# Performance work log

Measured on AMD Instinct MI355X. Metric: run time of the kernel, lower is better.

Reference implementation:

```python
import jax, jax.numpy as jnp
import numpy as np

D = 512      # d_model
H = 8        # n_heads
DH = D // H  # d_head
WIN = 128    # window radius
FF = 4 * D   # ffn hidden
B, T = 4, 2048
EPS = 1e-5


def _ln(x, g, b):
    mu = jnp.mean(x, axis=-1, keepdims=True)
    var = jnp.mean((x - mu) ** 2, axis=-1, keepdims=True)
    return (x - mu) * jax.lax.rsqrt(var + EPS) * g + b


def _rope(x):
    # standard rotate-half RoPE over the full d_model dim (applied to ln(x)
    # before q/k/v projections, as in the source module)
    t, d = x.shape[-2], x.shape[-1]
    half = d // 2
    inv_freq = 1.0 / (10000.0 ** (jnp.arange(half, dtype=jnp.float32) / half))
    ang = jnp.arange(t, dtype=jnp.float32)[:, None] * inv_freq[None, :]  # (T, half)
    cos, sin = jnp.cos(ang), jnp.sin(ang)
    x1, x2 = x[..., :half], x[..., half:]
    return jnp.concatenate([x1 * cos - x2 * sin, x1 * sin + x2 * cos], axis=-1)


def setup_inputs() -> dict:
    key = jax.random.key(0)
    ks = jax.random.split(key, 16)
    s = 0.02
    inp = {
        "x": jax.random.normal(ks[0], (B, T, D), dtype=jnp.float32),
        "Wq": jax.random.normal(ks[1], (D, D), dtype=jnp.float32) * s,
        "bq": jnp.zeros((D,), jnp.float32),
        "Wk": jax.random.normal(ks[2], (D, D), dtype=jnp.float32) * s,
        "bk": jnp.zeros((D,), jnp.float32),
        "Wv": jax.random.normal(ks[3], (D, D), dtype=jnp.float32) * s,
        "bv": jnp.zeros((D,), jnp.float32),
        "Wo": jax.random.normal(ks[4], (D, D), dtype=jnp.float32) * s,
        "bo": jnp.zeros((D,), jnp.float32),
        "ln_g": jnp.ones((D,), jnp.float32),
        "ln_b": jnp.zeros((D,), jnp.float32),
        "ffln_g": jnp.ones((D,), jnp.float32),
        "ffln_b": jnp.zeros((D,), jnp.float32),
        "W1": jax.random.normal(ks[5], (D, FF), dtype=jnp.float32) * s,
        "b1": jnp.zeros((FF,), jnp.float32),
        "W2": jax.random.normal(ks[6], (FF, D), dtype=jnp.float32) * s,
        "b2": jnp.zeros((D,), jnp.float32),
    }
    return inp


def reference(x, Wq, bq, Wk, bk, Wv, bv, Wo, bo, ln_g, ln_b, ffln_g, ffln_b, W1, b1, W2, b2):
    b, t, d = x.shape
    h = _rope(_ln(x, ln_g, ln_b))
    q = (h @ Wq + bq).reshape(b, t, H, DH).transpose(0, 2, 1, 3)  # (B,H,T,DH)
    k = (h @ Wk + bk).reshape(b, t, H, DH).transpose(0, 2, 1, 3)
    v = (h @ Wv + bv).reshape(b, t, H, DH).transpose(0, 2, 1, 3)

    scores = jnp.einsum("bhqd,bhkd->bhqk", q, k) / jnp.sqrt(jnp.float32(DH))
    # Faithful to source local_mask semantics under torch SDPA bool-mask
    # convention (True = attend): attention is ALLOWED where |i-j| > window.
    idx = jnp.arange(t)
    allowed = jnp.abs(idx[:, None] - idx[None, :]) > WIN  # (T,T) bool
    scores = jnp.where(allowed, scores, -jnp.inf)
    attn = jax.nn.softmax(scores, axis=-1)
    o = jnp.einsum("bhqk,bhkd->bhqd", attn, v)
    o = o.transpose(0, 2, 1, 3).reshape(b, t, d)
    x = x + (o @ Wo + bo)

    # source applies self.ln AND the ff's internal LayerNorm back-to-back
    f = _ln(_ln(x, ln_g, ln_b), ffln_g, ffln_b)
    f = jax.nn.gelu(f @ W1 + b1, approximate=False) @ W2 + b2
    return x + f
```

## Files before the change

### kernel.cpp

```cpp
#include <hip/hip_runtime.h>
#include <cmath>

typedef __bf16 bf16x8 __attribute__((ext_vector_type(8)));
typedef float  f32x4  __attribute__((ext_vector_type(4)));
typedef float  f32x16 __attribute__((ext_vector_type(16)));

#define MFMA(a, b, c)   __builtin_amdgcn_mfma_f32_16x16x32_bf16((a), (b), (c), 0, 0, 0)
#define MFMA32(a, b, c) __builtin_amdgcn_mfma_f32_32x32x16_bf16((a), (b), (c), 0, 0, 0)

static __device__ __forceinline__ __bf16 f2bf(float f) {
  union { float f; unsigned u; } v; v.f = f;
  unsigned r = v.u + 0x7fffu + ((v.u >> 16) & 1u);
  union { unsigned short u; __bf16 b; } o; o.u = (unsigned short)(r >> 16);
  return o.b;
}

typedef const __attribute__((address_space(1))) void* gas_t;
typedef __attribute__((address_space(3))) void* las_t;
static __device__ __forceinline__ void load_lds16(const __bf16* g, __bf16* l) {
  __builtin_amdgcn_global_load_lds((gas_t)g, (las_t)l, 16, 0, 0);
}

__global__ __launch_bounds__(256) void k_transpose_all(
    const float* __restrict__ Wq, const float* __restrict__ Wk,
    const float* __restrict__ Wv, const float* __restrict__ Wo,
    const float* __restrict__ W1, const float* __restrict__ W2,
    __bf16* __restrict__ wqkv, __bf16* __restrict__ wo,
    __bf16* __restrict__ w1t, __bf16* __restrict__ w2t) {
  int idx = blockIdx.x * 256 + threadIdx.x;
  const float* src; __bf16* dst; int off, logK, N;
  if (idx < 1048576) {
    int which = idx >> 18; off = idx & 262143; logK = 9; N = 512;
    src = which == 0 ? Wq : which == 1 ? Wk : which == 2 ? Wv : Wo;
    dst = which < 3 ? wqkv + which * 262144 : wo;
  } else if (idx < 2097152) {
    off = idx - 1048576; logK = 9; N = 2048; src = W1; dst = w1t;
  } else {
    off = idx - 2097152; logK = 11; N = 512; src = W2; dst = w2t;
  }
  int n = off >> logK, k = off & ((1 << logK) - 1);
  dst[off] = f2bf(src[(size_t)k * N + n]);
}

__global__ __launch_bounds__(256) void k_ln_rope(const float* __restrict__ x,
                                                 const float* __restrict__ g,
                                                 const float* __restrict__ b,
                                                 __bf16* __restrict__ h) {
  int n = blockIdx.x, tid = threadIdx.x;
  const float* row = x + (size_t)n * 512;
  float v1 = row[tid], v2 = row[tid + 256];
  float s = v1 + v2, ss = v1 * v1 + v2 * v2;
  #pragma unroll
  for (int off = 1; off < 64; off <<= 1) { s += __shfl_xor(s, off, 64); ss += __shfl_xor(ss, off, 64); }
  __shared__ float red[2][4];
  if ((tid & 63) == 0) { red[0][tid >> 6] = s; red[1][tid >> 6] = ss; }
  __syncthreads();
  s  = red[0][0] + red[0][1] + red[0][2] + red[0][3];
  ss = red[1][0] + red[1][1] + red[1][2] + red[1][3];
  float mu = s * (1.f / 512.f);
  float var = ss * (1.f / 512.f) - mu * mu;
  float rs = rsqrtf(var + 1e-5f);
  float y1 = (v1 - mu) * rs * g[tid] + b[tid];
  float y2 = (v2 - mu) * rs * g[tid + 256] + b[tid + 256];
  int t = n & 2047;
  float inv = __expf(-(float)tid * 0.03597789207803197f);
  float ang = (float)t * inv;
  float sn, c;
  __sincosf(ang, &sn, &c);
  h[(size_t)n * 512 + tid]       = f2bf(y1 * c - y2 * sn);
  h[(size_t)n * 512 + tid + 256] = f2bf(y1 * sn + y2 * c);
}

template <int K>
static __device__ __forceinline__ void gemm128(const __bf16* __restrict__ A,
                                               const __bf16* __restrict__ Bt,
                                               f32x4 (&acc)[2][4]) {
  __shared__ __bf16 lA[128 * 64];
  __shared__ __bf16 lB[128 * 64];
  int bm = blockIdx.x & 63, bn = blockIdx.x >> 6;
  int tid = threadIdx.x, w = tid >> 6, lane = tid & 63;
  int l16 = lane & 15, quad = lane >> 4;
  int wr = (w & 3) * 32, wc = (w >> 2) * 64;
  int srow = w * 8 + (lane >> 3);
  int sg = (lane & 7) ^ (srow & 7);
  const __bf16* ga = A  + (size_t)(bm * 128 + srow) * K + sg * 8;
  const __bf16* gb = Bt + (size_t)(bn * 128 + srow) * K + sg * 8;
  __bf16* saw = lA + w * 512;
  __bf16* sbw = lB + w * 512;
  #pragma unroll
  for (int i = 0; i < 2; ++i)
    #pragma unroll
    for (int j = 0; j < 4; ++j) acc[i][j] = {0.f, 0.f, 0.f, 0.f};
  const size_t rstep = (size_t)64 * K;
  for (int k0 = 0; k0 < K; k0 += 64) {
    load_lds16(ga + k0,         saw);
    load_lds16(ga + k0 + rstep, saw + 4096);
    load_lds16(gb + k0,         sbw);
    load_lds16(gb + k0 + rstep, sbw + 4096);
    __syncthreads();
    #pragma unroll
    for (int kk = 0; kk < 2; ++kk) {
      int gg = kk * 4 + quad;
      bf16x8 af[2], bfr[4];
      #pragma unroll
      for (int i = 0; i < 2; ++i) {
        int row = wr + i * 16 + l16;
        __builtin_memcpy(&af[i], &lA[row * 64 + ((gg ^ (row & 7)) * 8)], 16);
      }
      #pragma unroll
      for (int j = 0; j < 4; ++j) {
        int row = wc + j * 16 + l16;
        __builtin_memcpy(&bfr[j], &lB[row * 64 + ((gg ^ (row & 7)) * 8)], 16);
      }
      #pragma unroll
      for (int i = 0; i < 2; ++i)
        #pragma unroll
        for (int j = 0; j < 4; ++j) acc[i][j] = MFMA(af[i], bfr[j], acc[i][j]);
    }
    __syncthreads();
  }
}

#define G128_EPILOG_IDX                                 \
  int bm = blockIdx.x & 63, bn = blockIdx.x >> 6;       \
  int lane = threadIdx.x & 63, w = threadIdx.x >> 6;    \
  int l16 = lane & 15, quad = lane >> 4;                \
  int wr = (w & 3) * 32, wc = (w >> 2) * 64;

__global__ __launch_bounds__(512) void k_gemm_qkv(const __bf16* __restrict__ A,
                                                  const __bf16* __restrict__ Bt,
                                                  const float* __restrict__ bq,
                                                  const float* __restrict__ bk,
                                                  const float* __restrict__ bv,
                                                  __bf16* __restrict__ qo,
                                                  __bf16* __restrict__ ko,
                                                  __bf16* __restrict__ vT) {
  f32x4 acc[2][4];
  gemm128<512>(A, Bt, acc);
  G128_EPILOG_IDX
  int proj = bn >> 2;
  const float* bias = proj == 0 ? bq : (proj == 1 ? bk : bv);
  float scale = proj == 0 ? 0.125f : 1.f;
  if (proj < 2) {
    __bf16* dst = proj == 0 ? qo : ko;
    #pragma unroll
    for (int i = 0; i < 2; ++i)
      #pragma unroll
      for (int j = 0; j < 4; ++j)
        #pragma unroll
        for (int r = 0; r < 4; ++r) {
          int c = (bn * 128 + wc + j * 16 + l16) & 511;
          int m = bm * 128 + wr + i * 16 + quad * 4 + r;
          int bI = m >> 11, t = m & 2047;
          int head = c >> 6, dh = c & 63;
          dst[(((size_t)bI * 8 + head) * 2048 + t) * 64 + dh] = f2bf((acc[i][j][r] + bias[c]) * scale);
        }
  } else {
    #pragma unroll
    for (int i = 0; i < 2; ++i)
      #pragma unroll
      for (int j = 0; j < 4; ++j)
        #pragma unroll
        for (int r = 0; r < 4; ++r) {
          int c = (bn * 128 + wc + j * 16 + l16) & 511;
          int m = bm * 128 + wr + i * 16 + quad * 4 + r;
          int bI = m >> 11, t = m & 2047;
          int head = c >> 6, dh = c & 63;
          vT[(((size_t)bI * 8 + head) * 64 + dh) * 2048 + t] = f2bf(acc[i][j][r] + bias[c]);
        }
  }
}

__global__ __launch_bounds__(512) void k_attn(const __bf16* __restrict__ q,
                                              const __bf16* __restrict__ k,
                                              const __bf16* __restrict__ vT,
                                              __bf16* __restrict__ o) {
  __shared__ __align__(16) __bf16 Kt[64 * 64];
  __shared__ __align__(16) __bf16 Vt[64 * 64];
  __shared__ __align__(16) __bf16 P[8][32][40];
  __shared__ float cbuf[4][64][17];
  int bh = blockIdx.x >> 4, qblk = blockIdx.x & 15;
  int tid = threadIdx.x, w = tid >> 6, lane = tid & 63;
  int l32 = lane & 31, h32 = lane >> 5;
  int qw = w & 3, half = w >> 2, hoff = half * 32;
  int qB = qblk * 128;
  int q0 = qB + qw * 32;
  const __bf16* qb = q + (size_t)bh * 2048 * 64;
  const __bf16* kb = k + (size_t)bh * 2048 * 64;
  const __bf16* vb = vT + (size_t)bh * 64 * 2048;
  bf16x8 aq[4];
  #pragma unroll
  for (int i = 0; i < 4; ++i)
    aq[i] = *(const bf16x8*)(qb + (size_t)(q0 + l32) * 64 + i * 16 + h32 * 8);
  f32x16 on0 = {0,0,0,0,0,0,0,0,0,0,0,0,0,0,0,0};
  f32x16 on1 = {0,0,0,0,0,0,0,0,0,0,0,0,0,0,0,0};
  float lsum[16];
  #pragma unroll
  for (int i = 0; i < 16; ++i) lsum[i] = 0.f;
  int srow = w * 8 + (lane >> 3);
  int sg = (lane & 7) ^ (srow & 7);
  const __bf16* gk = kb + (size_t)srow * 64 + sg * 8;
  const __bf16* gv = vb + (size_t)srow * 2048 + sg * 8;
  __bf16* skw = Kt + w * 512;
  __bf16* svw = Vt + w * 512;

  for (int it = 0; it < 32; ++it) {
    int kt64 = it * 64;
    if ((unsigned)(kt64 - qB) <= 64u) continue;
    load_lds16(gk + (size_t)kt64 * 64, skw);
    load_lds16(gv + kt64, svw);
    __syncthreads();
    int myk0 = kt64 + hoff;
    bool skip = (q0 + 31 - myk0 <= 128) && (myk0 + 31 - q0 <= 128);
    if (!skip) {
      bool need_mask = !((myk0 >= q0 + 160) || (myk0 <= q0 - 160));
      f32x16 sc = {0,0,0,0,0,0,0,0,0,0,0,0,0,0,0,0};
      int krow = hoff + l32;
      #pragma unroll
      for (int i = 0; i < 4; ++i) {
        int gg = i * 2 + h32;
        bf16x8 bk;
        __builtin_memcpy(&bk, &Kt[krow * 64 + ((gg ^ (l32 & 7)) * 8)], 16);
        sc = MFMA32(aq[i], bk, sc);
      }
      #pragma unroll
      for (int reg = 0; reg < 16; ++reg) {
        int row = (reg & 3) + 8 * (reg >> 2) + 4 * h32;
        float p = __expf(sc[reg]);
        if (need_mask) {
          int qi = q0 + row, kj = myk0 + l32;
          if ((unsigned)(qi - kj + 128) <= 256u) p = 0.f;
        }
        P[w][row][l32] = f2bf(p);
        lsum[reg] += p;
      }
      bf16x8 ap0, ap1;
      __builtin_memcpy(&ap0, &P[w][l32][h32 * 8], 16);
      __builtin_memcpy(&ap1, &P[w][l32][16 + h32 * 8], 16);
      #pragma unroll
      for (int kk = 0; kk < 2; ++kk) {
        bf16x8 ap = kk ? ap1 : ap0;
        int gg = half * 4 + kk * 2 + h32;
        bf16x8 bv0, bv1;
        __builtin_memcpy(&bv0, &Vt[l32 * 64 + ((gg ^ (l32 & 7)) * 8)], 16);
        __builtin_memcpy(&bv1, &Vt[(32 + l32) * 64 + ((gg ^ (l32 & 7)) * 8)], 16);
        on0 = MFMA32(ap, bv0, on0);
        on1 = MFMA32(ap, bv1, on1);
      }
    }
    __syncthreads();
  }
  if (half) {
    for (int i = 0; i < 16; ++i) cbuf[qw][lane][i] = on0[i];
  }
  __syncthreads();
  if (!half) {
    for (int i = 0; i < 16; ++i) on0[i] += cbuf[qw][lane][i];
  }
  __syncthreads();
  if (half) {
    for (int i = 0; i < 16; ++i) cbuf[qw][lane][i] = on1[i];
  }
  __syncthreads();
  if (!half) {
    for (int i = 0; i < 16; ++i) on1[i] += cbuf[qw][lane][i];
  }
  __syncthreads();
  if (half) {
    for (int i = 0; i < 16; ++i) cbuf[qw][lane][i] = lsum[i];
  }
  __syncthreads();
  if (!half) {
    #pragma unroll
    for (int i = 0; i < 16; ++i) {
      float s = lsum[i] + cbuf[qw][lane][i];
      #pragma unroll
      for (int off = 1; off < 32; off <<= 1) s += __shfl_xor(s, off, 64);
      lsum[i] = 1.f / s;
    }
    int bI = bh >> 3, head = bh & 7;
    #pragma unroll
    for (int reg = 0; reg < 16; ++reg) {
      int row = (reg & 3) + 8 * (reg >> 2) + 4 * h32;
      size_t base = ((size_t)(bI * 2048 + q0 + row)) * 512 + head * 64;
      o[base + l32]      = f2bf(on0[reg] * lsum[reg]);
      o[base + 32 + l32] = f2bf(on1[reg] * lsum[reg]);
    }
  }
}

__global__ __launch_bounds__(512) void k_gemm_oproj(const __bf16* __restrict__ A,
                                                    const __bf16* __restrict__ Bt,
                                                    const float* __restrict__ bo,
                                                    const float* __restrict__ xin,
                                                    float* __restrict__ x2) {
  f32x4 acc[2][4];
  gemm128<512>(A, Bt, acc);
  G128_EPILOG_IDX
  #pragma unroll
  for (int i = 0; i < 2; ++i)
    #pragma unroll
    for (int j = 0; j < 4; ++j)
      #pragma unroll
      for (int r = 0; r < 4; ++r) {
        int n = bn * 128 + wc + j * 16 + l16;
        int m = bm * 128 + wr + i * 16 + quad * 4 + r;
        size_t idx = (size_t)m * 512 + n;
        x2[idx] = xin[idx] + acc[i][j][r] + bo[n];
      }
}

__global__ __launch_bounds__(256) void k_ln_ln(const float* __restrict__ x2,
                                               const float* __restrict__ g1v,
                                               const float* __restrict__ b1v,
                                               const float* __restrict__ g2v,
                                               const float* __restrict__ b2v,
                                               __bf16* __restrict__ fout) {
  int n = blockIdx.x, tid = threadIdx.x;
  const float* row = x2 + (size_t)n * 512;
  float v1 = row[tid], v2 = row[tid + 256];
  __shared__ float red[2][4];
  float s = v1 + v2, ss = v1 * v1 + v2 * v2;
  #pragma unroll
  for (int off = 1; off < 64; off <<= 1) { s += __shfl_xor(s, off, 64); ss += __shfl_xor(ss, off, 64); }
  if ((tid & 63) == 0) { red[0][tid >> 6] = s; red[1][tid >> 6] = ss; }
  __syncthreads();
  s  = red[0][0] + red[0][1] + red[0][2] + red[0][3];
  ss = red[1][0] + red[1][1] + red[1][2] + red[1][3];
  float mu = s * (1.f / 512.f), var = ss * (1.f / 512.f) - mu * mu;
  float rs = rsqrtf(var + 1e-5f);
  float y1 = (v1 - mu) * rs * g1v[tid] + b1v[tid];
  float y2 = (v2 - mu) * rs * g1v[tid + 256] + b1v[tid + 256];
  __syncthreads();
  s = y1 + y2; ss = y1 * y1 + y2 * y2;
  #pragma unroll
  for (int off = 1; off < 64; off <<= 1) { s += __shfl_xor(s, off, 64); ss += __shfl_xor(ss, off, 64); }
  if ((tid & 63) == 0) { red[0][tid >> 6] = s; red[1][tid >> 6] = ss; }
  __syncthreads();
  s  = red[0][0] + red[0][1] + red[0][2] + red[0][3];
  ss = red[1][0] + red[1][1] + red[1][2] + red[1][3];
  float mu2 = s * (1.f / 512.f), var2 = ss * (1.f / 512.f) - mu2 * mu2;
  float rs2 = rsqrtf(var2 + 1e-5f);
  fout[(size_t)n * 512 + tid]       = f2bf((y1 - mu2) * rs2 * g2v[tid] + b2v[tid]);
  fout[(size_t)n * 512 + tid + 256] = f2bf((y2 - mu2) * rs2 * g2v[tid + 256] + b2v[tid + 256]);
}

__global__ __launch_bounds__(512) void k_gemm_ffn1(const __bf16* __restrict__ A,
                                                   const __bf16* __restrict__ Bt,
                                                   const float* __restrict__ b1,
                                                   __bf16* __restrict__ g1) {
  f32x4 acc[2][4];
  gemm128<512>(A, Bt, acc);
  G128_EPILOG_IDX
  #pragma unroll
  for (int i = 0; i < 2; ++i)
    #pragma unroll
    for (int j = 0; j < 4; ++j)
      #pragma unroll
      for (int r = 0; r < 4; ++r) {
        int n = bn * 128 + wc + j * 16 + l16;
        int m = bm * 128 + wr + i * 16 + quad * 4 + r;
        float t = acc[i][j][r] + b1[n];
        float ge = 0.5f * t * (1.f + erff(t * 0.7071067811865475f));
        g1[(size_t)m * 2048 + n] = f2bf(ge);
      }
}

__global__ __launch_bounds__(512) void k_gemm_ffn2(const __bf16* __restrict__ A,
                                                   const __bf16* __restrict__ Bt,
                                                   const float* __restrict__ b2,
                                                   const float* __restrict__ x2,
                                                   float* __restrict__ out) {
  f32x4 acc[2][4];
  gemm128<2048>(A, Bt, acc);
  G128_EPILOG_IDX
  #pragma unroll
  for (int i = 0; i < 2; ++i)
    #pragma unroll
    for (int j = 0; j < 4; ++j)
      #pragma unroll
      for (int r = 0; r < 4; ++r) {
        int n = bn * 128 + wc + j * 16 + l16;
        int m = bm * 128 + wr + i * 16 + quad * 4 + r;
        size_t idx = (size_t)m * 512 + n;
        out[idx] = x2[idx] + acc[i][j][r] + b2[n];
      }
}

extern "C" void kernel_launch(void* const* d_in, const int* in_sizes, int n_in,
                              void* d_out, int out_size, void* d_ws, size_t ws_size,
                              hipStream_t stream) {
  (void)in_sizes; (void)n_in; (void)out_size; (void)ws_size;
  const float* x   = (const float*)d_in[0];
  const float* Wq  = (const float*)d_in[1];
  const float* bq  = (const float*)d_in[2];
  const float* Wk  = (const float*)d_in[3];
  const float* bk  = (const float*)d_in[4];
  const float* Wv  = (const float*)d_in[5];
  const float* bv  = (const float*)d_in[6];
  const float* Wo  = (const float*)d_in[7];
  const float* bo  = (const float*)d_in[8];
  const float* lng = (const float*)d_in[9];
  const float* lnb = (const float*)d_in[10];
  const float* ffg = (const float*)d_in[11];
  const float* ffb = (const float*)d_in[12];
  const float* W1  = (const float*)d_in[13];
  const float* b1  = (const float*)d_in[14];
  const float* W2  = (const float*)d_in[15];
  const float* b2  = (const float*)d_in[16];
  float* out = (float*)d_out;

  char* ws = (char*)d_ws;
  __bf16* h    = (__bf16*)(ws);
  __bf16* qb   = (__bf16*)(ws + (size_t)8 * 1024 * 1024);
  __bf16* kb   = (__bf16*)(ws + (size_t)16 * 1024 * 1024);
  __bf16* vT   = (__bf16*)(ws + (size_t)24 * 1024 * 1024);
  float*  x2   = (float*)(ws + (size_t)32 * 1024 * 1024);
  __bf16* fb   = (__bf16*)(ws + (size_t)48 * 1024 * 1024);
  __bf16* wqkv = (__bf16*)(ws + (size_t)56 * 1024 * 1024);
  __bf16* wo   = wqkv + 3 * 512 * 512;
  __bf16* w1t  = wo + 512 * 512;
  __bf16* w2t  = w1t + 512 * 2048;
  __bf16* g1   = (__bf16*)(ws);

  k_transpose_all<<<12288, 256, 0, stream>>>(Wq, Wk, Wv, Wo, W1, W2, wqkv, wo, w1t, w2t);
  k_ln_rope<<<8192, 256, 0, stream>>>(x, lng, lnb, h);
  k_gemm_qkv<<<64 * 12, 512, 0, stream>>>(h, wqkv, bq, bk, bv, qb, kb, vT);
  k_attn<<<32 * 16, 512, 0, stream>>>(qb, kb, vT, h);
  k_gemm_oproj<<<64 * 4, 512, 0, stream>>>(h, wo, bo, x, x2);
  k_ln_ln<<<8192, 256, 0, stream>>>(x2, lng, lnb, ffg, ffb, fb);
  k_gemm_ffn1<<<64 * 16, 512, 0, stream>>>(fb, w1t, b1, g1);
  k_gemm_ffn2<<<64 * 4, 512, 0, stream>>>(g1, w2t, b2, x2, out);
}
```

Measured before the change: 287.1 us.

## Use 64x64 split-K GEMM tiles for o-proj and FFN2, truncate P to bf16

Replaces the 128x128 tile GEMMs for the output projection and second FFN matmul with a 64x64 tile kernel. The eight waves are split into two halves over K, and the halves are reduced through shared memory. This raises the block count from 256 to 1024 so the N=512 GEMMs fill more compute units, at the cost of more redundant A/B loads and an LDS reduction. Separately, the attention P matrix now uses truncation instead of round-to-nearest bf16 conversion, which saves ALU work but adds a small rounding bias.

```diff
diff --git a/kernel.cpp b/kernel.cpp
--- a/kernel.cpp
+++ b/kernel.cpp
@@ -12,6 +12,11 @@
   union { float f; unsigned u; } v; v.f = f;
   unsigned r = v.u + 0x7fffu + ((v.u >> 16) & 1u);
   union { unsigned short u; __bf16 b; } o; o.u = (unsigned short)(r >> 16);
+  return o.b;
+}
+static __device__ __forceinline__ __bf16 f2bf_tr(float f) {
+  union { float f; unsigned u; } v; v.f = f;
+  union { unsigned short u; __bf16 b; } o; o.u = (unsigned short)(v.u >> 16);
   return o.b;
 }
 
@@ -169,6 +174,104 @@
           vT[(((size_t)bI * 8 + head) * 64 + dh) * 2048 + t] = f2bf(acc[i][j][r] + bias[c]);
         }
   }
+}
+
+template <int K, typename EPI>
+static __device__ __forceinline__ void gemm64sk(const __bf16* __restrict__ A,
+                                                const __bf16* __restrict__ Bt,
+                                                EPI epi) {
+  __shared__ __align__(16) char smem[64 * 128 * 2 * 2];
+  __bf16* lA = (__bf16*)smem;
+  __bf16* lB = lA + 64 * 128;
+  int bm = blockIdx.x & 127, bn = blockIdx.x >> 7;
+  int tid = threadIdx.x, w = tid >> 6, lane = tid & 63;
+  int l16 = lane & 15, quad = lane >> 4;
+  int pos = w & 3, half = w >> 2;
+  int wr = (pos >> 1) * 32, wc = (pos & 1) * 32;
+  int srow = tid >> 4;
+  int sg = (tid & 15) ^ (srow & 15);
+  const __bf16* ga = A  + (size_t)(bm * 64 + srow) * K + sg * 8;
+  const __bf16* gb = Bt + (size_t)(bn * 64 + srow) * K + sg * 8;
+  __bf16* sa = lA + w * 512;
+  __bf16* sb = lB + w * 512;
+  f32x4 acc[2][2];
+  #pragma unroll
+  for (int i = 0; i < 2; ++i)
+    #pragma unroll
+    for (int j = 0; j < 2; ++j) acc[i][j] = {0.f, 0.f, 0.f, 0.f};
+  const size_t rstep = (size_t)32 * K;
+  for (int k0 = 0; k0 < K; k0 += 128) {
+    load_lds16(ga + k0,         sa);
+    load_lds16(ga + k0 + rstep, sa + 4096);
+    load_lds16(gb + k0,         sb);
+    load_lds16(gb + k0 + rstep, sb + 4096);
+    __syncthreads();
+    #pragma unroll
+    for (int kk = 0; kk < 2; ++kk) {
+      int gg = half * 8 + kk * 4 + quad;
+      bf16x8 af[2], bfr[2];
+      #pragma unroll
+      for (int i = 0; i < 2; ++i) {
+        int row = wr + i * 16 + l16;
+        __builtin_memcpy(&af[i], &lA[row * 128 + ((gg ^ (row & 15)) * 8)], 16);
+      }
+      #pragma unroll
+      for (int j = 0; j < 2; ++j) {
+        int row = wc + j * 16 + l16;
+        __builtin_memcpy(&bfr[j], &lB[row * 128 + ((gg ^ (row & 15)) * 8)], 16);
+      }
+      #pragma unroll
+      for (int i = 0; i < 2; ++i)
+        #pragma unroll
+        for (int j = 0; j < 2; ++j) acc[i][j] = MFMA(af[i], bfr[j], acc[i][j]);
+    }
+    __syncthreads();
+  }
+  float (*cbuf)[64][17] = (float(*)[64][17])smem;
+  if (half) {
+    #pragma unroll
+    for (int i = 0; i < 2; ++i)
+      #pragma unroll
+      for (int j = 0; j < 2; ++j)
+        #pragma unroll
+        for (int r = 0; r < 4; ++r) cbuf[pos][lane][(i * 2 + j) * 4 + r] = acc[i][j][r];
+  }
+  __syncthreads();
+  if (!half) {
+    #pragma unroll
+    for (int i = 0; i < 2; ++i)
+      #pragma unroll
+      for (int j = 0; j < 2; ++j)
+        #pragma unroll
+        for (int r = 0; r < 4; ++r) {
+          float v = acc[i][j][r] + cbuf[pos][lane][(i * 2 + j) * 4 + r];
+          int m = bm * 64 + wr + i * 16 + quad * 4 + r;
+          int n = bn * 64 + wc + j * 16 + l16;
+          epi(m, n, v);
+        }
+  }
+}
+
+__global__ __launch_bounds__(512) void k_gemm_oproj(const __bf16* __restrict__ A,
+                                                    const __bf16* __restrict__ Bt,
+                                                    const float* __restrict__ bo,
+                                                    const float* __restrict__ xin,
+                                                    float* __restrict__ x2) {
+  gemm64sk<512>(A, Bt, [&](int m, int n, float v) {
+    size_t idx = (size_t)m * 512 + n;
+    x2[idx] = xin[idx] + v + bo[n];
+  });
+}
+
+__global__ __launch_bounds__(512) void k_gemm_ffn2(const __bf16* __restrict__ A,
+                                                   const __bf16* __restrict__ Bt,
+                                                   const float* __restrict__ b2,
+                                                   const float* __restrict__ x2,
+                                                   float* __restrict__ out) {
+  gemm64sk<2048>(A, Bt, [&](int m, int n, float v) {
+    size_t idx = (size_t)m * 512 + n;
+    out[idx] = x2[idx] + v + b2[n];
+  });
 }
 
 __global__ __launch_bounds__(512) void k_attn(const __bf16* __restrict__ q,
@@ -231,7 +334,7 @@
           int qi = q0 + row, kj = myk0 + l32;
           if ((unsigned)(qi - kj + 128) <= 256u) p = 0.f;
         }
-        P[w][row][l32] = f2bf(p);
+        P[w][row][l32] = f2bf_tr(p);
         lsum[reg] += p;
       }
       bf16x8 ap0, ap1;
@@ -287,27 +390,6 @@
       o[base + 32 + l32] = f2bf(on1[reg] * lsum[reg]);
     }
   }
-}
-
-__global__ __launch_bounds__(512) void k_gemm_oproj(const __bf16* __restrict__ A,
-                                                    const __bf16* __restrict__ Bt,
-                                                    const float* __restrict__ bo,
-                                                    const float* __restrict__ xin,
-                                                    float* __restrict__ x2) {
-  f32x4 acc[2][4];
-  gemm128<512>(A, Bt, acc);
-  G128_EPILOG_IDX
-  #pragma unroll
-  for (int i = 0; i < 2; ++i)
-    #pragma unroll
-    for (int j = 0; j < 4; ++j)
-      #pragma unroll
-      for (int r = 0; r < 4; ++r) {
-        int n = bn * 128 + wc + j * 16 + l16;
-        int m = bm * 128 + wr + i * 16 + quad * 4 + r;
-        size_t idx = (size_t)m * 512 + n;
-        x2[idx] = xin[idx] + acc[i][j][r] + bo[n];
-      }
 }
 
 __global__ __launch_bounds__(256) void k_ln_ln(const float* __restrict__ x2,
@@ -363,27 +445,6 @@
         float t = acc[i][j][r] + b1[n];
         float ge = 0.5f * t * (1.f + erff(t * 0.7071067811865475f));
         g1[(size_t)m * 2048 + n] = f2bf(ge);
-      }
-}
-
-__global__ __launch_bounds__(512) void k_gemm_ffn2(const __bf16* __restrict__ A,
-                                                   const __bf16* __restrict__ Bt,
-                                                   const float* __restrict__ b2,
-                                                   const float* __restrict__ x2,
-                                                   float* __restrict__ out) {
-  f32x4 acc[2][4];
-  gemm128<2048>(A, Bt, acc);
-  G128_EPILOG_IDX
-  #pragma unroll
-  for (int i = 0; i < 2; ++i)
-    #pragma unroll
-    for (int j = 0; j < 4; ++j)
-      #pragma unroll
-      for (int r = 0; r < 4; ++r) {
-        int n = bn * 128 + wc + j * 16 + l16;
-        int m = bm * 128 + wr + i * 16 + quad * 4 + r;
-        size_t idx = (size_t)m * 512 + n;
-        out[idx] = x2[idx] + acc[i][j][r] + b2[n];
       }
 }
 
@@ -427,8 +488,8 @@
   k_ln_rope<<<8192, 256, 0, stream>>>(x, lng, lnb, h);
   k_gemm_qkv<<<64 * 12, 512, 0, stream>>>(h, wqkv, bq, bk, bv, qb, kb, vT);
   k_attn<<<32 * 16, 512, 0, stream>>>(qb, kb, vT, h);
-  k_gemm_oproj<<<64 * 4, 512, 0, stream>>>(h, wo, bo, x, x2);
+  k_gemm_oproj<<<128 * 8, 512, 0, stream>>>(h, wo, bo, x, x2);
   k_ln_ln<<<8192, 256, 0, stream>>>(x2, lng, lnb, ffg, ffb, fb);
   k_gemm_ffn1<<<64 * 16, 512, 0, stream>>>(fb, w1t, b1, g1);
-  k_gemm_ffn2<<<64 * 4, 512, 0, stream>>>(g1, w2t, b2, x2, out);
-}
+  k_gemm_ffn2<<<128 * 8, 512, 0, stream>>>(g1, w2t, b2, x2, out);
+}
```

Measured after the change: 277.1 us. 1.04x faster.
